# Performance work log

Hardware: AMD Instinct MI355X
Metric: run time of the kernel (lower is better)

## Reference

```python
import jax, jax.numpy as jnp
import numpy as np

COMMITMENT_COST = 0.25
LAMBDA_KL = 1.0
EPS = 1e-10


def setup_inputs() -> dict:
    key = jax.random.key(0)
    k1, k2 = jax.random.split(key)
    x = jax.random.normal(k1, (8, 4096, 256), dtype=jnp.float32)
    embedding = jax.random.normal(k2, (1024, 256), dtype=jnp.float32)
    return {"x": x, "embedding": embedding}


def reference(x, embedding):
    B, T, D = x.shape
    M, _ = embedding.shape
    x_sg = jax.lax.stop_gradient(x)
    x_flat = x_sg.reshape(-1, D)  # [N, D]
    distances = (jnp.sum(embedding ** 2, axis=1)[None, :]
                 + jnp.sum(x_flat ** 2, axis=1, keepdims=True)
                 - 2.0 * (x_flat @ embedding.T))  # [N, M]
    indices = jnp.argmin(distances.astype(jnp.float32), axis=-1)  # [N]
    quantized = embedding[indices].reshape(B, T, D)
    # losses (x detached in both terms, matching torch)
    loss = (COMMITMENT_COST * jnp.mean((x_sg - quantized) ** 2)
            + jnp.mean((quantized - x_sg) ** 2)) * LAMBDA_KL
    # straight-through estimator
    quantized_st = x + jax.lax.stop_gradient(quantized - x)
    # avg of one-hot encodings == normalized code counts (avoids NxM one-hot)
    N = B * T
    counts = jnp.zeros((M,), dtype=jnp.float32).at[indices].add(1.0)
    avg_probs = counts / N
    perplexity = jnp.exp(-jnp.sum(avg_probs * jnp.log(avg_probs + EPS)))
    return (quantized_st, loss, indices.reshape(B, T), perplexity)
```

## Files before the change

### kernel.cpp

```cpp
#include <hip/hip_runtime.h>


constexpr int D = 256;
constexpr int M = 1024;
constexpr int ROWS = 64;

typedef _Float16 f16;
typedef __attribute__((ext_vector_type(8)))  _Float16 f16x8;
typedef __attribute__((ext_vector_type(4)))  float f32x4;
typedef __attribute__((ext_vector_type(16))) float f32x16;

constexpr size_t WS_ENORM_F = 1028;
constexpr size_t WS_TAB_B   = 8320;
constexpr size_t WS_NEEDED  = 1056896;

__device__ inline void gload_lds16(const void* g, void* l) {
    __builtin_amdgcn_global_load_lds(
        (const __attribute__((address_space(1))) unsigned int*)(g),
        (__attribute__((address_space(3))) unsigned int*)(l), 16, 0, 0);
}

__global__ __launch_bounds__(256) void prep_kernel(const float* __restrict__ e,
                                                   float* __restrict__ ws) {
    const int b = blockIdx.x, t = threadIdx.x;
    if (b < 256) {
        int v    = b * 256 + t;
        int lane = v & 63, u = (v >> 6) & 15;
        int ksl  = (v >> 10) & 1, t32 = v >> 11;
        int kstep = u & 7, spl = u >> 3;
        int row  = t32 * 32 + (lane & 31);
        int col0 = (ksl * 8 + kstep) * 16 + (lane >> 5) * 8;
        const float* p = e + (size_t)row * D + col0;
        f32x4 a = *reinterpret_cast<const f32x4*>(p);
        f32x4 c = *reinterpret_cast<const f32x4*>(p + 4);
        f16 h0=(f16)a.x,h1=(f16)a.y,h2=(f16)a.z,h3=(f16)a.w;
        f16 h4=(f16)c.x,h5=(f16)c.y,h6=(f16)c.z,h7=(f16)c.w;
        f16x8 out;
        if (spl == 0) out = (f16x8){h0,h1,h2,h3,h4,h5,h6,h7};
        else          out = (f16x8){(f16)(a.x-(float)h0),(f16)(a.y-(float)h1),
                                    (f16)(a.z-(float)h2),(f16)(a.w-(float)h3),
                                    (f16)(c.x-(float)h4),(f16)(c.y-(float)h5),
                                    (f16)(c.z-(float)h6),(f16)(c.w-(float)h7)};
        *reinterpret_cast<f16x8*>((char*)ws + WS_TAB_B + (size_t)v * 16) = out;
    } else if (b < 512) {
        int row  = (b - 256) * 4 + (t >> 6);
        int lane = t & 63;
        f32x4 a = *reinterpret_cast<const f32x4*>(e + (size_t)row * D + lane * 4);
        float s = fmaf(a.x, a.x, fmaf(a.y, a.y, fmaf(a.z, a.z, a.w * a.w)));
#pragma unroll
        for (int o = 32; o > 0; o >>= 1) s += __shfl_down(s, o, 64);
        if (lane == 0) ws[WS_ENORM_F + row] = s;
    } else {
        for (int i = t; i < 1026; i += 256) ws[i] = 0.f;
    }
}

__global__ __launch_bounds__(256, 2) void vq_fused_kernel(
    const float* __restrict__ x, const float* __restrict__ e,
    float* __restrict__ outQ, float* __restrict__ outIdx, float* __restrict__ ws)
{
    __shared__ ushort ebuf[2][2][8192];
    __shared__ float  en_s[M];
    __shared__ float  wval[4][32];
    __shared__ int    widx[4][32];
    __shared__ float  xns[ROWS];
    __shared__ int    fidx[ROWS];

    const int tid   = threadIdx.x;
    const int w     = __builtin_amdgcn_readfirstlane(tid >> 6);
    const int l     = tid & 63;
    const int rpair = w >> 1;
    const int mhalf = w & 1;
    const int R     = blockIdx.x * ROWS;
    const int xr    = l & 31;
    const int kg    = l >> 5;
    const char* tab = (const char*)ws + WS_TAB_B;

    auto stage = [&](int buf, int g) {
        int tt = g >> 1, ks = g & 1;
#pragma unroll
        for (int i = 0; i < 8; ++i) {
            int S = w * 8 + i, half = S >> 4, sg = S & 15;
            gload_lds16(tab + (size_t)(((half * 16 + tt) * 2 + ks)) * 16384 + sg * 1024 + l * 16,
                        &ebuf[buf][half][sg * 512]);
        }
    };
    stage(0, 0);

    {
        f32x4 v = *reinterpret_cast<const f32x4*>(ws + WS_ENORM_F + tid * 4);
        *reinterpret_cast<f32x4*>(&en_s[tid * 4]) = v;
    }

    f16x8 Xh[16], Xl[16];
    float xn;
    {
        float s = 0.f;
#pragma unroll
        for (int ku = 0; ku < 16; ++ku) {
            const float* p = x + (size_t)(R + rpair * 32 + xr) * D + ku * 16 + kg * 8;
            f32x4 a = *reinterpret_cast<const f32x4*>(p);
            f32x4 c = *reinterpret_cast<const f32x4*>(p + 4);
            f16 h0=(f16)a.x,h1=(f16)a.y,h2=(f16)a.z,h3=(f16)a.w;
            f16 h4=(f16)c.x,h5=(f16)c.y,h6=(f16)c.z,h7=(f16)c.w;
            Xh[ku] = (f16x8){h0,h1,h2,h3,h4,h5,h6,h7};
            Xl[ku] = (f16x8){(f16)(a.x-(float)h0),(f16)(a.y-(float)h1),
                             (f16)(a.z-(float)h2),(f16)(a.w-(float)h3),
                             (f16)(c.x-(float)h4),(f16)(c.y-(float)h5),
                             (f16)(c.z-(float)h6),(f16)(c.w-(float)h7)};
            s = fmaf(a.x,a.x,fmaf(a.y,a.y,fmaf(a.z,a.z,fmaf(a.w,a.w,
                fmaf(c.x,c.x,fmaf(c.y,c.y,fmaf(c.z,c.z,fmaf(c.w,c.w,s))))))));
        }
        s += __shfl_xor(s, 32, 64);
        xn = s;
    }
    __syncthreads();

    float bV = 3.4e38f;
    int   bI = 0;
    const ushort* eb0 = &ebuf[0][mhalf][0];
    const ushort* eb1 = &ebuf[1][mhalf][0];

    for (int t = 0; t < 16; ++t) {
        f32x16 accA = {0.f}, accB = {0.f}, accC = {0.f};

        stage(1, 2 * t + 1);
        __builtin_amdgcn_s_setprio(1);
#pragma unroll
        for (int kstep = 0; kstep < 8; ++kstep) {
            f16x8 Ah = *reinterpret_cast<const f16x8*>(eb0 + kstep * 512 + l * 8);
            f16x8 Al = *reinterpret_cast<const f16x8*>(eb0 + (8 + kstep) * 512 + l * 8);
            accA = __builtin_amdgcn_mfma_f32_32x32x16_f16(Ah, Xh[kstep], accA, 0, 0, 0);
            accB = __builtin_amdgcn_mfma_f32_32x32x16_f16(Al, Xh[kstep], accB, 0, 0, 0);
            accC = __builtin_amdgcn_mfma_f32_32x32x16_f16(Ah, Xl[kstep], accC, 0, 0, 0);
        }
        __builtin_amdgcn_s_setprio(0);
        __syncthreads();

        if (t < 15) stage(0, 2 * t + 2);
        __builtin_amdgcn_s_setprio(1);
#pragma unroll
        for (int kstep = 0; kstep < 8; ++kstep) {
            f16x8 Ah = *reinterpret_cast<const f16x8*>(eb1 + kstep * 512 + l * 8);
            f16x8 Al = *reinterpret_cast<const f16x8*>(eb1 + (8 + kstep) * 512 + l * 8);
            accA = __builtin_amdgcn_mfma_f32_32x32x16_f16(Ah, Xh[8 + kstep], accA, 0, 0, 0);
            accB = __builtin_amdgcn_mfma_f32_32x32x16_f16(Al, Xh[8 + kstep], accB, 0, 0, 0);
            accC = __builtin_amdgcn_mfma_f32_32x32x16_f16(Ah, Xl[8 + kstep], accC, 0, 0, 0);
        }
        __builtin_amdgcn_s_setprio(0);
        __syncthreads();

        const int mbase = mhalf * 512 + t * 32;
#pragma unroll
        for (int rq = 0; rq < 4; ++rq) {
            f32x4 en4 = *reinterpret_cast<const f32x4*>(&en_s[mbase + rq * 8 + kg * 4]);
#pragma unroll
            for (int j = 0; j < 4; ++j) {
                int reg = rq * 4 + j;
                int mi  = mbase + rq * 8 + kg * 4 + j;
                float dv = fmaf(-2.f, accA[reg] + accB[reg] + accC[reg], en4[j]);
                if (dv < bV) { bV = dv; bI = mi; }
            }
        }
    }

    {
        float ov = __shfl_xor(bV, 32, 64);
        int   oi = __shfl_xor(bI, 32, 64);
        if (ov < bV || (ov == bV && oi < bI)) { bV = ov; bI = oi; }
    }
    if (l < 32) {
        wval[w][xr] = bV;
        widx[w][xr] = bI;
        if (mhalf == 0) xns[rpair * 32 + xr] = xn;
    }
    __syncthreads();

    if (tid < 64) {
        int r = tid, g2 = r >> 5, rr = r & 31;
        float v0 = wval[g2 * 2 + 0][rr]; int i0 = widx[g2 * 2 + 0][rr];
        float v1 = wval[g2 * 2 + 1][rr]; int i1 = widx[g2 * 2 + 1][rr];
        float fv; int fi;
        if (v1 < v0) { fv = v1; fi = i1; } else { fv = v0; fi = i0; }
        fidx[r] = fi;
        outIdx[R + r] = (float)fi;
        atomicAdd(ws + 1 + fi, 1.0f);
        float ls = fv + xns[r];
#pragma unroll
        for (int o = 32; o > 0; o >>= 1) ls += __shfl_down(ls, o, 64);
        if (r == 0) atomicAdd(ws, ls);
    }
    __syncthreads();

#pragma unroll
    for (int it = 0; it < 16; ++it) {
        int u = it * 256 + tid;
        int row = u >> 6, c4 = u & 63;
        f32x4 v = *reinterpret_cast<const f32x4*>(e + (size_t)fidx[row] * D + c4 * 4);
        __builtin_nontemporal_store(v, reinterpret_cast<f32x4*>(outQ + (size_t)(R + row) * D + c4 * 4));
    }
}

__global__ void enorm_kernel(const float* __restrict__ e, float* __restrict__ enorm) {
    int m = blockIdx.x, l = threadIdx.x;
    const f32x4 v = *reinterpret_cast<const f32x4*>(e + m * D + l * 4);
    float s = fmaf(v.x, v.x, fmaf(v.y, v.y, fmaf(v.z, v.z, v.w * v.w)));
#pragma unroll
    for (int o = 32; o > 0; o >>= 1) s += __shfl_down(s, o, 64);
    if (l == 0) enorm[m] = s;
}

__global__ __launch_bounds__(256, 2) void vq_main_kernel(
    const float* __restrict__ x, const float* __restrict__ e,
    float* __restrict__ outQ, float* __restrict__ outIdx, float* __restrict__ ws) {
    __shared__ f32x4 xs[64][64];
    __shared__ float cval[4][64];
    __shared__ int   cidx[4][64];
    __shared__ int   fidx[64];
    const int tid = threadIdx.x, row0 = blockIdx.x * 64;
#pragma unroll
    for (int it = 0; it < 16; ++it) {
        int f = it * 256 + tid, rr = f >> 6, c4 = f & 63;
        xs[rr][c4 ^ (rr & 7)] = *reinterpret_cast<const f32x4*>(x + (row0 + rr) * D + c4 * 4);
    }
    __syncthreads();
    const int r = tid & 63, c = __builtin_amdgcn_readfirstlane(tid >> 6), sw = r & 7;
    float xnorm = 0.f;
    if (c == 0) {
        f32x4 a = (f32x4){0.f,0.f,0.f,0.f};
        for (int d4 = 0; d4 < 64; ++d4) {
            f32x4 xv = xs[r][d4 ^ sw];
            a.x = fmaf(xv.x, xv.x, a.x); a.y = fmaf(xv.y, xv.y, a.y);
            a.z = fmaf(xv.z, xv.z, a.z); a.w = fmaf(xv.w, xv.w, a.w);
        }
        xnorm = (a.x + a.y) + (a.z + a.w);
    }
    const float* __restrict__ enorm = ws + WS_ENORM_F;
    float bestVal = 3.4e38f; int bestIdx = 0;
    for (int chunk = 0; chunk < M / 32; ++chunk) {
        const int m0 = chunk * 32 + c * 8;
        f32x4 acc[8];
#pragma unroll
        for (int mi = 0; mi < 8; ++mi) acc[mi] = (f32x4){0.f,0.f,0.f,0.f};
#pragma unroll 2
        for (int d4 = 0; d4 < 64; ++d4) {
            const f32x4 xv = xs[r][d4 ^ sw];
#pragma unroll
            for (int mi = 0; mi < 8; ++mi) {
                const f32x4 ev = *reinterpret_cast<const f32x4*>(e + (m0 + mi) * D + d4 * 4);
                acc[mi].x = fmaf(xv.x, ev.x, acc[mi].x); acc[mi].y = fmaf(xv.y, ev.y, acc[mi].y);
                acc[mi].z = fmaf(xv.z, ev.z, acc[mi].z); acc[mi].w = fmaf(xv.w, ev.w, acc[mi].w);
            }
        }
#pragma unroll
        for (int mi = 0; mi < 8; ++mi) {
            float dot = (acc[mi].x + acc[mi].y) + (acc[mi].z + acc[mi].w);
            float val = enorm[m0 + mi] - 2.0f * dot;
            if (val < bestVal) { bestVal = val; bestIdx = m0 + mi; }
        }
    }
    cval[c][r] = bestVal; cidx[c][r] = bestIdx;
    __syncthreads();
    if (c == 0) {
        float bv = bestVal; int bi = bestIdx;
#pragma unroll
        for (int cc = 1; cc < 4; ++cc) {
            float v = cval[cc][r]; int i = cidx[cc][r];
            if (v < bv || (v == bv && i < bi)) { bv = v; bi = i; }
        }
        fidx[r] = bi; outIdx[row0 + r] = (float)bi;
        atomicAdd(ws + 1 + bi, 1.0f);
        float dist = bv + xnorm;
#pragma unroll
        for (int o = 32; o > 0; o >>= 1) dist += __shfl_down(dist, o, 64);
        if (r == 0) atomicAdd(ws, dist);
    }
    __syncthreads();
#pragma unroll
    for (int it = 0; it < 16; ++it) {
        int f = it * 256 + tid, rr = f >> 6, c4 = f & 63;
        *reinterpret_cast<f32x4*>(outQ + (row0 + rr) * D + c4 * 4) =
            *reinterpret_cast<const f32x4*>(e + fidx[rr] * D + c4 * 4);
    }
}

__global__ void vq_final_kernel(const float* __restrict__ ws,
                                float* __restrict__ outLoss, float* __restrict__ outPpl,
                                float invN, float invND) {
    int t = threadIdx.x;
    float p = ws[1 + t] * invN;
    float term = p * logf(p + 1e-10f);
#pragma unroll
    for (int o = 32; o > 0; o >>= 1) term += __shfl_down(term, o, 64);
    __shared__ float s[16];
    if ((t & 63) == 0) s[t >> 6] = term;
    __syncthreads();
    if (t == 0) {
        float tot = 0.f;
#pragma unroll
        for (int i = 0; i < 16; ++i) tot += s[i];
        *outPpl  = expf(-tot);
        *outLoss = 1.25f * ws[0] * invND;
    }
}

extern "C" void kernel_launch(void* const* d_in, const int* in_sizes, int n_in,
                              void* d_out, int out_size, void* d_ws, size_t ws_size,
                              hipStream_t stream) {
    const float* x = (const float*)d_in[0];
    const float* e = (const float*)d_in[1];
    const int NX = in_sizes[0];
    const int N  = NX / D;

    float* out     = (float*)d_out;
    float* outQ    = out;
    float* outLoss = out + NX;
    float* outIdx  = out + NX + 1;
    float* outPpl  = out + NX + 1 + N;
    float* ws      = (float*)d_ws;

    if (ws_size >= WS_NEEDED && (N % ROWS) == 0) {
        prep_kernel<<<513, 256, 0, stream>>>(e, ws);
        vq_fused_kernel<<<N / ROWS, 256, 0, stream>>>(x, e, outQ, outIdx, ws);
    } else {
        (void)hipMemsetAsync(d_ws, 0, 4112, stream);
        enorm_kernel<<<M, 64, 0, stream>>>(e, ws + WS_ENORM_F);
        vq_main_kernel<<<N / 64, 256, 0, stream>>>(x, e, outQ, outIdx, ws);
    }
    vq_final_kernel<<<1, 1024, 0, stream>>>(ws, outLoss, outPpl,
                                            1.0f / (float)N, 1.0f / (float)NX);
}
```

Before: 79.89 us.

## Use 512-thread blocks of 128 rows with triple-buffered codebook staging

Doubles rows per block to 128 with 8 waves, so each codebook tile staged in LDS is shared by twice as many rows. The double buffer becomes a three-slot ring with prefetch distance two, using explicit vmcnt waits and a single barrier per stage instead of two syncthreads. This halves block count and relies on one block per CU, trading occupancy and more LDS for better reuse and fewer barriers.

```diff
diff --git a/kernel.cpp b/kernel.cpp
--- a/kernel.cpp
+++ b/kernel.cpp
@@ -3,7 +3,7 @@
 
 constexpr int D = 256;
 constexpr int M = 1024;
-constexpr int ROWS = 64;
+constexpr int ROWS = 128;
 
 typedef _Float16 f16;
 typedef __attribute__((ext_vector_type(8)))  _Float16 f16x8;
@@ -55,14 +55,14 @@
     }
 }
 
-__global__ __launch_bounds__(256, 2) void vq_fused_kernel(
+__global__ __launch_bounds__(512, 1) void vq_fused_kernel(
     const float* __restrict__ x, const float* __restrict__ e,
     float* __restrict__ outQ, float* __restrict__ outIdx, float* __restrict__ ws)
 {
-    __shared__ ushort ebuf[2][2][8192];
+    __shared__ ushort ebuf[3][2][8192];
     __shared__ float  en_s[M];
-    __shared__ float  wval[4][32];
-    __shared__ int    widx[4][32];
+    __shared__ float  wval[8][32];
+    __shared__ int    widx[8][32];
     __shared__ float  xns[ROWS];
     __shared__ int    fidx[ROWS];
 
@@ -79,15 +79,14 @@
     auto stage = [&](int buf, int g) {
         int tt = g >> 1, ks = g & 1;
 #pragma unroll
-        for (int i = 0; i < 8; ++i) {
-            int S = w * 8 + i, half = S >> 4, sg = S & 15;
+        for (int i = 0; i < 4; ++i) {
+            int S = w * 4 + i, half = S >> 4, sg = S & 15;
             gload_lds16(tab + (size_t)(((half * 16 + tt) * 2 + ks)) * 16384 + sg * 1024 + l * 16,
                         &ebuf[buf][half][sg * 512]);
         }
     };
-    stage(0, 0);
-
-    {
+
+    if (tid < 256) {
         f32x4 v = *reinterpret_cast<const f32x4*>(ws + WS_ENORM_F + tid * 4);
         *reinterpret_cast<f32x4*>(&en_s[tid * 4]) = v;
     }
@@ -114,54 +113,66 @@
         s += __shfl_xor(s, 32, 64);
         xn = s;
     }
-    __syncthreads();
+
+    __builtin_amdgcn_sched_barrier(0);
+    stage(0, 0);
+    stage(1, 1);
+    asm volatile("s_waitcnt lgkmcnt(0)" ::: "memory");
 
     float bV = 3.4e38f;
     int   bI = 0;
-    const ushort* eb0 = &ebuf[0][mhalf][0];
-    const ushort* eb1 = &ebuf[1][mhalf][0];
-
-    for (int t = 0; t < 16; ++t) {
-        f32x16 accA = {0.f}, accB = {0.f}, accC = {0.f};
-
-        stage(1, 2 * t + 1);
-        __builtin_amdgcn_s_setprio(1);
-#pragma unroll
-        for (int kstep = 0; kstep < 8; ++kstep) {
-            f16x8 Ah = *reinterpret_cast<const f16x8*>(eb0 + kstep * 512 + l * 8);
-            f16x8 Al = *reinterpret_cast<const f16x8*>(eb0 + (8 + kstep) * 512 + l * 8);
-            accA = __builtin_amdgcn_mfma_f32_32x32x16_f16(Ah, Xh[kstep], accA, 0, 0, 0);
-            accB = __builtin_amdgcn_mfma_f32_32x32x16_f16(Al, Xh[kstep], accB, 0, 0, 0);
-            accC = __builtin_amdgcn_mfma_f32_32x32x16_f16(Ah, Xl[kstep], accC, 0, 0, 0);
-        }
-        __builtin_amdgcn_s_setprio(0);
-        __syncthreads();
-
-        if (t < 15) stage(0, 2 * t + 2);
-        __builtin_amdgcn_s_setprio(1);
-#pragma unroll
-        for (int kstep = 0; kstep < 8; ++kstep) {
-            f16x8 Ah = *reinterpret_cast<const f16x8*>(eb1 + kstep * 512 + l * 8);
-            f16x8 Al = *reinterpret_cast<const f16x8*>(eb1 + (8 + kstep) * 512 + l * 8);
-            accA = __builtin_amdgcn_mfma_f32_32x32x16_f16(Ah, Xh[8 + kstep], accA, 0, 0, 0);
-            accB = __builtin_amdgcn_mfma_f32_32x32x16_f16(Al, Xh[8 + kstep], accB, 0, 0, 0);
-            accC = __builtin_amdgcn_mfma_f32_32x32x16_f16(Ah, Xl[8 + kstep], accC, 0, 0, 0);
-        }
-        __builtin_amdgcn_s_setprio(0);
-        __syncthreads();
-
-        const int mbase = mhalf * 512 + t * 32;
-#pragma unroll
-        for (int rq = 0; rq < 4; ++rq) {
-            f32x4 en4 = *reinterpret_cast<const f32x4*>(&en_s[mbase + rq * 8 + kg * 4]);
-#pragma unroll
-            for (int j = 0; j < 4; ++j) {
-                int reg = rq * 4 + j;
-                int mi  = mbase + rq * 8 + kg * 4 + j;
-                float dv = fmaf(-2.f, accA[reg] + accB[reg] + accC[reg], en4[j]);
-                if (dv < bV) { bV = dv; bI = mi; }
+    f32x16 accA, accB, accC;
+    int cb = 0;
+
+    for (int g = 0; g < 32; ++g) {
+        if (g < 31) asm volatile("s_waitcnt vmcnt(4)" ::: "memory");
+        else        asm volatile("s_waitcnt vmcnt(0)" ::: "memory");
+        __builtin_amdgcn_s_barrier();
+
+        if (g + 2 < 32) {
+            int pb = cb + 2; if (pb >= 3) pb -= 3;
+            stage(pb, g + 2);
+        }
+
+        const ushort* eb = &ebuf[cb][mhalf][0];
+        if ((g & 1) == 0) {
+            accA = (f32x16){0.f}; accB = (f32x16){0.f}; accC = (f32x16){0.f};
+            __builtin_amdgcn_s_setprio(1);
+#pragma unroll
+            for (int kstep = 0; kstep < 8; ++kstep) {
+                f16x8 Ah = *reinterpret_cast<const f16x8*>(eb + kstep * 512 + l * 8);
+                f16x8 Al = *reinterpret_cast<const f16x8*>(eb + (8 + kstep) * 512 + l * 8);
+                accA = __builtin_amdgcn_mfma_f32_32x32x16_f16(Ah, Xh[kstep], accA, 0, 0, 0);
+                accB = __builtin_amdgcn_mfma_f32_32x32x16_f16(Al, Xh[kstep], accB, 0, 0, 0);
+                accC = __builtin_amdgcn_mfma_f32_32x32x16_f16(Ah, Xl[kstep], accC, 0, 0, 0);
             }
-        }
+            __builtin_amdgcn_s_setprio(0);
+        } else {
+            __builtin_amdgcn_s_setprio(1);
+#pragma unroll
+            for (int kstep = 0; kstep < 8; ++kstep) {
+                f16x8 Ah = *reinterpret_cast<const f16x8*>(eb + kstep * 512 + l * 8);
+                f16x8 Al = *reinterpret_cast<const f16x8*>(eb + (8 + kstep) * 512 + l * 8);
+                accA = __builtin_amdgcn_mfma_f32_32x32x16_f16(Ah, Xh[8 + kstep], accA, 0, 0, 0);
+                accB = __builtin_amdgcn_mfma_f32_32x32x16_f16(Al, Xh[8 + kstep], accB, 0, 0, 0);
+                accC = __builtin_amdgcn_mfma_f32_32x32x16_f16(Ah, Xl[8 + kstep], accC, 0, 0, 0);
+            }
+            __builtin_amdgcn_s_setprio(0);
+
+            const int mbase = mhalf * 512 + (g >> 1) * 32;
+#pragma unroll
+            for (int rq = 0; rq < 4; ++rq) {
+                f32x4 en4 = *reinterpret_cast<const f32x4*>(&en_s[mbase + rq * 8 + kg * 4]);
+#pragma unroll
+                for (int j = 0; j < 4; ++j) {
+                    int reg = rq * 4 + j;
+                    int mi  = mbase + rq * 8 + kg * 4 + j;
+                    float dv = fmaf(-2.f, accA[reg] + accB[reg] + accC[reg], en4[j]);
+                    if (dv < bV) { bV = dv; bI = mi; }
+                }
+            }
+        }
+        cb = cb + 1; if (cb >= 3) cb -= 3;
     }
 
     {
@@ -176,7 +187,7 @@
     }
     __syncthreads();
 
-    if (tid < 64) {
+    if (tid < ROWS) {
         int r = tid, g2 = r >> 5, rr = r & 31;
         float v0 = wval[g2 * 2 + 0][rr]; int i0 = widx[g2 * 2 + 0][rr];
         float v1 = wval[g2 * 2 + 1][rr]; int i1 = widx[g2 * 2 + 1][rr];
@@ -188,13 +199,13 @@
         float ls = fv + xns[r];
 #pragma unroll
         for (int o = 32; o > 0; o >>= 1) ls += __shfl_down(ls, o, 64);
-        if (r == 0) atomicAdd(ws, ls);
+        if ((r & 63) == 0) atomicAdd(ws, ls);
     }
     __syncthreads();
 
 #pragma unroll
     for (int it = 0; it < 16; ++it) {
-        int u = it * 256 + tid;
+        int u = it * 512 + tid;
         int row = u >> 6, c4 = u & 63;
         f32x4 v = *reinterpret_cast<const f32x4*>(e + (size_t)fidx[row] * D + c4 * 4);
         __builtin_nontemporal_store(v, reinterpret_cast<f32x4*>(outQ + (size_t)(R + row) * D + c4 * 4));
@@ -321,7 +332,7 @@
 
     if (ws_size >= WS_NEEDED && (N % ROWS) == 0) {
         prep_kernel<<<513, 256, 0, stream>>>(e, ws);
-        vq_fused_kernel<<<N / ROWS, 256, 0, stream>>>(x, e, outQ, outIdx, ws);
+        vq_fused_kernel<<<N / ROWS, 512, 0, stream>>>(x, e, outQ, outIdx, ws);
     } else {
         (void)hipMemsetAsync(d_ws, 0, 4112, stream);
         enorm_kernel<<<M, 64, 0, stream>>>(e, ws + WS_ENORM_F);
```

New measurement: 90.58 us. 1.13x slower.

## Halve rows per block to 32 with 2 waves and finer 4-phase K pipeline

Applied to the files above, without the earlier changes.

Blocks now cover 32 rows with two waves, each wave taking half of the codebook, instead of 64 rows with four waves. The codebook staging is reorganized into four K-slices per tile with double buffering, and the prep kernel's table layout changes to match. This doubles the grid to improve occupancy and load balance and shrinks LDS per block. In exchange, each block re-streams the whole codebook for half as many rows, doubling total L2-to-LDS traffic, and adds more barriers per tile.

```diff
diff --git a/kernel.cpp b/kernel.cpp
--- a/kernel.cpp
+++ b/kernel.cpp
@@ -3,7 +3,7 @@
 
 constexpr int D = 256;
 constexpr int M = 1024;
-constexpr int ROWS = 64;
+constexpr int ROWS = 32;
 
 typedef _Float16 f16;
 typedef __attribute__((ext_vector_type(8)))  _Float16 f16x8;
@@ -25,11 +25,11 @@
     const int b = blockIdx.x, t = threadIdx.x;
     if (b < 256) {
         int v    = b * 256 + t;
-        int lane = v & 63, u = (v >> 6) & 15;
-        int ksl  = (v >> 10) & 1, t32 = v >> 11;
-        int kstep = u & 7, spl = u >> 3;
+        int lane = v & 63, u = (v >> 6) & 7;
+        int kslice = (v >> 9) & 3, t32 = v >> 11;
+        int kstepp = u & 3, spl = u >> 2;
         int row  = t32 * 32 + (lane & 31);
-        int col0 = (ksl * 8 + kstep) * 16 + (lane >> 5) * 8;
+        int col0 = (kslice * 4 + kstepp) * 16 + (lane >> 5) * 8;
         const float* p = e + (size_t)row * D + col0;
         f32x4 a = *reinterpret_cast<const f32x4*>(p);
         f32x4 c = *reinterpret_cast<const f32x4*>(p + 4);
@@ -55,41 +55,38 @@
     }
 }
 
-__global__ __launch_bounds__(256, 2) void vq_fused_kernel(
+__global__ __launch_bounds__(128, 2) void vq_fused_kernel(
     const float* __restrict__ x, const float* __restrict__ e,
     float* __restrict__ outQ, float* __restrict__ outIdx, float* __restrict__ ws)
 {
-    __shared__ ushort ebuf[2][2][8192];
+    __shared__ ushort ebuf[2][2][4096];
     __shared__ float  en_s[M];
-    __shared__ float  wval[4][32];
-    __shared__ int    widx[4][32];
-    __shared__ float  xns[ROWS];
+    __shared__ float  wval[2][32];
+    __shared__ int    widx[2][32];
     __shared__ int    fidx[ROWS];
 
-    const int tid   = threadIdx.x;
-    const int w     = __builtin_amdgcn_readfirstlane(tid >> 6);
-    const int l     = tid & 63;
-    const int rpair = w >> 1;
-    const int mhalf = w & 1;
-    const int R     = blockIdx.x * ROWS;
-    const int xr    = l & 31;
-    const int kg    = l >> 5;
+    const int tid = threadIdx.x;
+    const int w   = __builtin_amdgcn_readfirstlane(tid >> 6);
+    const int l   = tid & 63;
+    const int xr  = l & 31;
+    const int kg  = l >> 5;
+    const int R   = blockIdx.x * ROWS;
     const char* tab = (const char*)ws + WS_TAB_B;
 
-    auto stage = [&](int buf, int g) {
-        int tt = g >> 1, ks = g & 1;
-#pragma unroll
-        for (int i = 0; i < 8; ++i) {
-            int S = w * 8 + i, half = S >> 4, sg = S & 15;
-            gload_lds16(tab + (size_t)(((half * 16 + tt) * 2 + ks)) * 16384 + sg * 1024 + l * 16,
-                        &ebuf[buf][half][sg * 512]);
-        }
+    auto stage = [&](int buf, int phase) {
+        int tt = phase >> 2, ks = phase & 3;
+        const char* src = tab + (size_t)(((w * 16 + tt) * 4) + ks) * 8192;
+#pragma unroll
+        for (int i = 0; i < 8; ++i)
+            gload_lds16(src + i * 1024 + l * 16, &ebuf[buf][w][i * 512]);
     };
     stage(0, 0);
 
     {
-        f32x4 v = *reinterpret_cast<const f32x4*>(ws + WS_ENORM_F + tid * 4);
-        *reinterpret_cast<f32x4*>(&en_s[tid * 4]) = v;
+        f32x4 v0 = *reinterpret_cast<const f32x4*>(ws + WS_ENORM_F + tid * 8);
+        f32x4 v1 = *reinterpret_cast<const f32x4*>(ws + WS_ENORM_F + tid * 8 + 4);
+        *reinterpret_cast<f32x4*>(&en_s[tid * 8])     = v0;
+        *reinterpret_cast<f32x4*>(&en_s[tid * 8 + 4]) = v1;
     }
 
     f16x8 Xh[16], Xl[16];
@@ -98,7 +95,7 @@
         float s = 0.f;
 #pragma unroll
         for (int ku = 0; ku < 16; ++ku) {
-            const float* p = x + (size_t)(R + rpair * 32 + xr) * D + ku * 16 + kg * 8;
+            const float* p = x + (size_t)(R + xr) * D + ku * 16 + kg * 8;
             f32x4 a = *reinterpret_cast<const f32x4*>(p);
             f32x4 c = *reinterpret_cast<const f32x4*>(p + 4);
             f16 h0=(f16)a.x,h1=(f16)a.y,h2=(f16)a.z,h3=(f16)a.w;
@@ -118,39 +115,29 @@
 
     float bV = 3.4e38f;
     int   bI = 0;
-    const ushort* eb0 = &ebuf[0][mhalf][0];
-    const ushort* eb1 = &ebuf[1][mhalf][0];
 
     for (int t = 0; t < 16; ++t) {
         f32x16 accA = {0.f}, accB = {0.f}, accC = {0.f};
-
-        stage(1, 2 * t + 1);
-        __builtin_amdgcn_s_setprio(1);
-#pragma unroll
-        for (int kstep = 0; kstep < 8; ++kstep) {
-            f16x8 Ah = *reinterpret_cast<const f16x8*>(eb0 + kstep * 512 + l * 8);
-            f16x8 Al = *reinterpret_cast<const f16x8*>(eb0 + (8 + kstep) * 512 + l * 8);
-            accA = __builtin_amdgcn_mfma_f32_32x32x16_f16(Ah, Xh[kstep], accA, 0, 0, 0);
-            accB = __builtin_amdgcn_mfma_f32_32x32x16_f16(Al, Xh[kstep], accB, 0, 0, 0);
-            accC = __builtin_amdgcn_mfma_f32_32x32x16_f16(Ah, Xl[kstep], accC, 0, 0, 0);
-        }
-        __builtin_amdgcn_s_setprio(0);
-        __syncthreads();
-
-        if (t < 15) stage(0, 2 * t + 2);
-        __builtin_amdgcn_s_setprio(1);
-#pragma unroll
-        for (int kstep = 0; kstep < 8; ++kstep) {
-            f16x8 Ah = *reinterpret_cast<const f16x8*>(eb1 + kstep * 512 + l * 8);
-            f16x8 Al = *reinterpret_cast<const f16x8*>(eb1 + (8 + kstep) * 512 + l * 8);
-            accA = __builtin_amdgcn_mfma_f32_32x32x16_f16(Ah, Xh[8 + kstep], accA, 0, 0, 0);
-            accB = __builtin_amdgcn_mfma_f32_32x32x16_f16(Al, Xh[8 + kstep], accB, 0, 0, 0);
-            accC = __builtin_amdgcn_mfma_f32_32x32x16_f16(Ah, Xl[8 + kstep], accC, 0, 0, 0);
-        }
-        __builtin_amdgcn_s_setprio(0);
-        __syncthreads();
-
-        const int mbase = mhalf * 512 + t * 32;
+#pragma unroll
+        for (int ks = 0; ks < 4; ++ks) {
+            const int phase = t * 4 + ks;
+            if (phase + 1 < 64) stage((ks + 1) & 1, phase + 1);
+
+            const ushort* eb = &ebuf[ks & 1][w][0];
+            __builtin_amdgcn_s_setprio(1);
+#pragma unroll
+            for (int kp = 0; kp < 4; ++kp) {
+                f16x8 Ah = *reinterpret_cast<const f16x8*>(eb + kp * 512 + l * 8);
+                f16x8 Al = *reinterpret_cast<const f16x8*>(eb + (4 + kp) * 512 + l * 8);
+                accA = __builtin_amdgcn_mfma_f32_32x32x16_f16(Ah, Xh[ks * 4 + kp], accA, 0, 0, 0);
+                accB = __builtin_amdgcn_mfma_f32_32x32x16_f16(Al, Xh[ks * 4 + kp], accB, 0, 0, 0);
+                accC = __builtin_amdgcn_mfma_f32_32x32x16_f16(Ah, Xl[ks * 4 + kp], accC, 0, 0, 0);
+            }
+            __builtin_amdgcn_s_setprio(0);
+            __syncthreads();
+        }
+
+        const int mbase = w * 512 + t * 32;
 #pragma unroll
         for (int rq = 0; rq < 4; ++rq) {
             f32x4 en4 = *reinterpret_cast<const f32x4*>(&en_s[mbase + rq * 8 + kg * 4]);
@@ -172,29 +159,26 @@
     if (l < 32) {
         wval[w][xr] = bV;
         widx[w][xr] = bI;
-        if (mhalf == 0) xns[rpair * 32 + xr] = xn;
-    }
-    __syncthreads();
-
-    if (tid < 64) {
-        int r = tid, g2 = r >> 5, rr = r & 31;
-        float v0 = wval[g2 * 2 + 0][rr]; int i0 = widx[g2 * 2 + 0][rr];
-        float v1 = wval[g2 * 2 + 1][rr]; int i1 = widx[g2 * 2 + 1][rr];
+    }
+    __syncthreads();
+
+    if (tid < 32) {
+        float v1 = wval[1][tid]; int i1 = widx[1][tid];
         float fv; int fi;
-        if (v1 < v0) { fv = v1; fi = i1; } else { fv = v0; fi = i0; }
-        fidx[r] = fi;
-        outIdx[R + r] = (float)fi;
+        if (v1 < bV) { fv = v1; fi = i1; } else { fv = bV; fi = bI; }
+        fidx[tid] = fi;
+        outIdx[R + tid] = (float)fi;
         atomicAdd(ws + 1 + fi, 1.0f);
-        float ls = fv + xns[r];
-#pragma unroll
-        for (int o = 32; o > 0; o >>= 1) ls += __shfl_down(ls, o, 64);
-        if (r == 0) atomicAdd(ws, ls);
+        float ls = fv + xn;
+#pragma unroll
+        for (int o = 16; o > 0; o >>= 1) ls += __shfl_down(ls, o, 32);
+        if (tid == 0) atomicAdd(ws, ls);
     }
     __syncthreads();
 
 #pragma unroll
     for (int it = 0; it < 16; ++it) {
-        int u = it * 256 + tid;
+        int u = it * 128 + tid;
         int row = u >> 6, c4 = u & 63;
         f32x4 v = *reinterpret_cast<const f32x4*>(e + (size_t)fidx[row] * D + c4 * 4);
         __builtin_nontemporal_store(v, reinterpret_cast<f32x4*>(outQ + (size_t)(R + row) * D + c4 * 4));
@@ -321,7 +305,7 @@
 
     if (ws_size >= WS_NEEDED && (N % ROWS) == 0) {
         prep_kernel<<<513, 256, 0, stream>>>(e, ws);
-        vq_fused_kernel<<<N / ROWS, 256, 0, stream>>>(x, e, outQ, outIdx, ws);
+        vq_fused_kernel<<<N / ROWS, 128, 0, stream>>>(x, e, outQ, outIdx, ws);
     } else {
         (void)hipMemsetAsync(d_ws, 0, 4112, stream);
         enorm_kernel<<<M, 64, 0, stream>>>(e, ws + WS_ENORM_F);
```

Measured after the change: 92.64 us. 1.16x slower.
